# Kernel optimization log

Hardware: AMD Instinct MI355X
Metric: run time of the kernel (lower is better)

## Reference

```python
import jax, jax.numpy as jnp
import numpy as np

D_MODEL = 1024
N_HEADS = 16
B, T = 16, 512


def setup_inputs() -> dict:
    key = jax.random.key(0)
    ks = jax.random.split(key, 5)
    s = 0.02
    return {
        "x": jax.random.normal(ks[0], (B, T, D_MODEL), dtype=jnp.float32),
        "w_qkv": jax.random.normal(ks[1], (D_MODEL, 3 * D_MODEL), dtype=jnp.float32) * s,
        "b_qkv": jax.random.normal(ks[2], (3 * D_MODEL,), dtype=jnp.float32) * s,
        "w_o": jax.random.normal(ks[3], (D_MODEL, D_MODEL), dtype=jnp.float32) * s,
        "b_o": jax.random.normal(ks[4], (D_MODEL,), dtype=jnp.float32) * s,
    }


def reference(x, w_qkv, b_qkv, w_o, b_o):
    Bx, Tx, C = x.shape
    H = N_HEADS
    hd = C // H
    qkv = x @ w_qkv + b_qkv                      # [B,T,3C]
    qkv = qkv.reshape(Bx, Tx, 3, H, hd).transpose(2, 0, 3, 1, 4)  # [3,B,H,T,hd]
    q, k, v = qkv[0], qkv[1], qkv[2]
    # NOTE: original scales by sqrt(C) = sqrt(d_model), not sqrt(head_dim)
    att = jnp.einsum("bhqd,bhkd->bhqk", q, k) / jnp.sqrt(jnp.float32(C))
    causal = jnp.tril(jnp.ones((Tx, Tx), dtype=bool))
    att = jnp.where(causal, att, -jnp.inf)
    att = jax.nn.softmax(att, axis=-1)
    y = jnp.einsum("bhqk,bhkd->bhqd", att, v)    # [B,H,T,hd]
    y = y.transpose(0, 2, 1, 3).reshape(Bx, Tx, C)
    return y @ w_o + b_o
```

## Files before the change

kernel.cpp:

```cpp
#include <hip/hip_runtime.h>
#include <cstddef>


#define B_  16
#define T_  512
#define C_  1024
#define H_  16
#define HD_ 64

typedef __bf16 bf16x8 __attribute__((ext_vector_type(8)));
typedef float  f32x4  __attribute__((ext_vector_type(4)));

__device__ __forceinline__ void gload16(const void* g, void* lds_dst) {
  __builtin_amdgcn_global_load_lds(
      (const __attribute__((address_space(1))) unsigned int*)g,
      (__attribute__((address_space(3))) unsigned int*)lds_dst, 16, 0, 0);
}

__global__ void cvt_kernel(const float* __restrict__ in, __bf16* __restrict__ out, int n) {
  int i = (blockIdx.x * 256 + threadIdx.x) * 8;
  if (i >= n) return;
  float4 f0 = *(const float4*)&in[i];
  float4 f1 = *(const float4*)&in[i + 4];
  bf16x8 o;
  o[0] = (__bf16)f0.x; o[1] = (__bf16)f0.y; o[2] = (__bf16)f0.z; o[3] = (__bf16)f0.w;
  o[4] = (__bf16)f1.x; o[5] = (__bf16)f1.y; o[6] = (__bf16)f1.z; o[7] = (__bf16)f1.w;
  *(bf16x8*)&out[i] = o;
}

__global__ void tconv_kernel(const float* __restrict__ w, __bf16* __restrict__ wt,
                             int K, int N) {
  __shared__ float tile[32][33];
  int tx = threadIdx.x, ty = threadIdx.y;
  int n0 = blockIdx.x * 32, k0 = blockIdx.y * 32;
  #pragma unroll
  for (int i = 0; i < 4; ++i) {
    int r = ty + i * 8;
    tile[r][tx] = w[(size_t)(k0 + r) * N + n0 + tx];
  }
  __syncthreads();
  #pragma unroll
  for (int i = 0; i < 4; ++i) {
    int r = ty + i * 8;
    wt[(size_t)(n0 + r) * K + k0 + tx] = (__bf16)tile[tx][r];
  }
}

__global__ __launch_bounds__(256) void gemmsq_kernel(
    const __bf16* __restrict__ A, const __bf16* __restrict__ BT,
    const float* __restrict__ bias, int K, int NBn,
    __bf16* __restrict__ oq, __bf16* __restrict__ okk, __bf16* __restrict__ ovt)
{
  __shared__ __attribute__((aligned(16))) char lds[32768];
  const int tid = threadIdx.x, lane = tid & 63, wid = tid >> 6;
  const int wm = wid >> 1, wn = wid & 1;
  const int lr = lane & 15, lg = lane >> 4;

  const int cpx = gridDim.x >> 3;
  const int id = (blockIdx.x & 7) * cpx + (blockIdx.x >> 3);
  const int m0 = (id / NBn) * 128, n0 = (id % NBn) * 128;

  const int r8  = wid * 8 + (lane >> 3);
  const int csw = ((lane & 7) ^ (lane >> 3)) * 8;

  auto stage = [&](const __bf16* g, char* dst) {
    #pragma unroll
    for (int i = 0; i < 4; ++i)
      gload16(g + (size_t)(i * 32 + r8) * K + csw, dst + i * 4096 + wid * 1024);
  };
  auto rd = [&](bf16x8* d, const char* buf, int woff) {
    #pragma unroll
    for (int f = 0; f < 4; ++f) {
      const char* rp = buf + (woff + f * 16 + lr) * 128;
      #pragma unroll
      for (int ks = 0; ks < 2; ++ks)
        d[f * 2 + ks] = *(const bf16x8*)(rp + (((ks << 2) + lg) ^ (lr & 7)) * 16);
    }
  };

  f32x4 acc[4][4] = {};
  const int nt = K >> 6;
  const __bf16* gA = A  + (size_t)m0 * K;
  const __bf16* gB = BT + (size_t)n0 * K;
  char* const Ab = lds;
  char* const Bb = lds + 16384;

  stage(gA, Ab);
  stage(gB, Bb);
  asm volatile("s_waitcnt vmcnt(0)\ns_barrier" ::: "memory");

  bf16x8 a[8], b[8];
  for (int t = 0; t < nt; ++t) {
    rd(a, Ab, wm * 64);
    rd(b, Bb, wn * 64);
    asm volatile("s_waitcnt lgkmcnt(0)\ns_barrier" ::: "memory");
    if (t + 1 < nt) {
      stage(gA + (size_t)(t + 1) * 64, Ab);
      stage(gB + (size_t)(t + 1) * 64, Bb);
    }
    __builtin_amdgcn_s_setprio(1);
    #pragma unroll
    for (int mf = 0; mf < 4; ++mf)
      #pragma unroll
      for (int nf = 0; nf < 4; ++nf)
        #pragma unroll
        for (int ks = 0; ks < 2; ++ks)
          acc[mf][nf] = __builtin_amdgcn_mfma_f32_16x16x32_bf16(
              a[mf * 2 + ks], b[nf * 2 + ks], acc[mf][nf], 0, 0, 0);
    __builtin_amdgcn_s_setprio(0);
    asm volatile("s_waitcnt vmcnt(0)\ns_barrier" ::: "memory");
  }

  const float QSC = 0.04508422f;
  #pragma unroll
  for (int nf = 0; nf < 4; ++nf) {
    int n = n0 + wn * 64 + nf * 16 + lr;
    float bv = bias[n];
    int which = n >> 10;
    int h = (n >> 6) & 15, d = n & 63;
    if (which == 2) {
      #pragma unroll
      for (int mf = 0; mf < 4; ++mf) {
        int m = m0 + wm * 64 + mf * 16 + lg * 4;
        int bb = m >> 9, t0 = m & 511;
        ushort4 pk;
        __bf16 e0 = (__bf16)(acc[mf][nf][0] + bv);
        __bf16 e1 = (__bf16)(acc[mf][nf][1] + bv);
        __bf16 e2 = (__bf16)(acc[mf][nf][2] + bv);
        __bf16 e3 = (__bf16)(acc[mf][nf][3] + bv);
        pk.x = *(unsigned short*)&e0; pk.y = *(unsigned short*)&e1;
        pk.z = *(unsigned short*)&e2; pk.w = *(unsigned short*)&e3;
        *(ushort4*)&ovt[(size_t)((bb * H_ + h) * HD_ + d) * T_ + t0] = pk;
      }
    } else {
      __bf16* dst = (which == 0) ? oq : okk;
      const float scl = (which == 0) ? QSC : 1.0f;
      #pragma unroll
      for (int mf = 0; mf < 4; ++mf)
        #pragma unroll
        for (int j = 0; j < 4; ++j) {
          int m = m0 + wm * 64 + mf * 16 + lg * 4 + j;
          int bb = m >> 9, tt = m & 511;
          dst[(size_t)((bb * H_ + h) * T_ + tt) * HD_ + d] =
              (__bf16)((acc[mf][nf][j] + bv) * scl);
        }
    }
  }
}

__global__ __launch_bounds__(256) void gemmsq_o_kernel(
    const __bf16* __restrict__ A, const __bf16* __restrict__ BT,
    const float* __restrict__ bias, int K, int NBn, int N,
    float* __restrict__ out32)
{
  __shared__ __attribute__((aligned(16))) char lds[32768];
  const int tid = threadIdx.x, lane = tid & 63, wid = tid >> 6;
  const int wm = wid >> 1, wn = wid & 1;
  const int lr = lane & 15, lg = lane >> 4;

  const int cpx = gridDim.x >> 3;
  const int id = (blockIdx.x & 7) * cpx + (blockIdx.x >> 3);
  const int m0 = (id / NBn) * 128, n0 = (id % NBn) * 128;

  const int r8  = wid * 8 + (lane >> 3);
  const int csw = ((lane & 7) ^ (lane >> 3)) * 8;

  auto stage = [&](const __bf16* g, char* dst) {
    #pragma unroll
    for (int i = 0; i < 4; ++i)
      gload16(g + (size_t)(i * 32 + r8) * K + csw, dst + i * 4096 + wid * 1024);
  };
  auto rd = [&](bf16x8* d, const char* buf, int woff) {
    #pragma unroll
    for (int f = 0; f < 4; ++f) {
      const char* rp = buf + (woff + f * 16 + lr) * 128;
      #pragma unroll
      for (int ks = 0; ks < 2; ++ks)
        d[f * 2 + ks] = *(const bf16x8*)(rp + (((ks << 2) + lg) ^ (lr & 7)) * 16);
    }
  };

  f32x4 acc[4][4] = {};
  const int nt = K >> 6;
  const __bf16* gA = A  + (size_t)m0 * K;
  const __bf16* gB = BT + (size_t)n0 * K;
  char* const Ab = lds;
  char* const Bb = lds + 16384;

  stage(gA, Ab);
  stage(gB, Bb);
  asm volatile("s_waitcnt vmcnt(0)\ns_barrier" ::: "memory");

  bf16x8 a[8], b[8];
  for (int t = 0; t < nt; ++t) {
    rd(a, Ab, wm * 64);
    rd(b, Bb, wn * 64);
    asm volatile("s_waitcnt lgkmcnt(0)\ns_barrier" ::: "memory");
    if (t + 1 < nt) {
      stage(gA + (size_t)(t + 1) * 64, Ab);
      stage(gB + (size_t)(t + 1) * 64, Bb);
    }
    __builtin_amdgcn_s_setprio(1);
    #pragma unroll
    for (int mf = 0; mf < 4; ++mf)
      #pragma unroll
      for (int nf = 0; nf < 4; ++nf)
        #pragma unroll
        for (int ks = 0; ks < 2; ++ks)
          acc[mf][nf] = __builtin_amdgcn_mfma_f32_16x16x32_bf16(
              a[mf * 2 + ks], b[nf * 2 + ks], acc[mf][nf], 0, 0, 0);
    __builtin_amdgcn_s_setprio(0);
    asm volatile("s_waitcnt vmcnt(0)\ns_barrier" ::: "memory");
  }

  #pragma unroll
  for (int nf = 0; nf < 4; ++nf) {
    int n = n0 + wn * 64 + nf * 16 + lr;
    float bv = bias[n];
    #pragma unroll
    for (int mf = 0; mf < 4; ++mf)
      #pragma unroll
      for (int j = 0; j < 4; ++j) {
        int m = m0 + wm * 64 + mf * 16 + lg * 4 + j;
        out32[(size_t)m * N + n] = acc[mf][nf][j] + bv;
      }
  }
}

__global__ __launch_bounds__(512) void attn_kernel(
    const __bf16* __restrict__ qb, const __bf16* __restrict__ kb,
    const __bf16* __restrict__ vtb, __bf16* __restrict__ y)
{
  extern __shared__ __align__(16) char smem[];
  char* const Ksb = smem;
  char* const Vtb = smem + 65536;
  __bf16* const Ps = (__bf16*)(smem + 131072);

  const int tid = threadIdx.x, lane = tid & 63, w = tid >> 6;
  const int lr = lane & 15, lg = lane >> 4;
  const int bh = blockIdx.x;
  const size_t base = (size_t)bh * T_ * HD_;
  const int b = bh >> 4, h = bh & 15;

  {
    const int rk = tid >> 3;
    const int sk = (tid & 7) ^ (rk & 7);
    const int rv = tid >> 6;
    const int sv = (tid & 63) ^ rv;
    #pragma unroll
    for (int i = 0; i < 8; ++i) {
      gload16(kb  + base + (size_t)(i * 64 + rk) * HD_ + sk * 8,
              Ksb + i * 8192 + w * 1024);
      gload16(vtb + base + (size_t)(i * 8 + rv) * T_ + sv * 8,
              Vtb + i * 8192 + w * 1024);
    }
  }
  asm volatile("s_waitcnt vmcnt(0)\ns_barrier" ::: "memory");

  bf16x8 onesf;
  #pragma unroll
  for (int i = 0; i < 8; ++i) onesf[i] = (__bf16)1.0f;

  #pragma unroll 1
  for (int k = 0; k < 4; ++k) {
    const int G = w + 8 * k;
    const int q0 = G * 16;
    const int cG = G >> 2;

    bf16x8 qf[2];
    #pragma unroll
    for (int s = 0; s < 2; ++s)
      qf[s] = *(const bf16x8*)&qb[base + (size_t)(q0 + lr) * HD_ + s * 32 + lg * 8];

    f32x4 acc[4] = {};
    f32x4 sacc = {};

    for (int c = 0; c <= cG; ++c) {
      f32x4 sc[4] = {};
      __builtin_amdgcn_s_setprio(1);
      #pragma unroll
      for (int s = 0; s < 2; ++s) {
        #pragma unroll
        for (int cc = 0; cc < 4; ++cc) {
          const char* kp = Ksb + (size_t)(c * 64 + cc * 16 + lr) * 128
                               + (((s << 2) + lg) ^ (lr & 7)) * 16;
          bf16x8 kf = *(const bf16x8*)kp;
          sc[cc] = __builtin_amdgcn_mfma_f32_16x16x32_bf16(qf[s], kf, sc[cc], 0, 0, 0);
        }
      }
      __builtin_amdgcn_s_setprio(0);

      #pragma unroll
      for (int cc = 0; cc < 4; ++cc)
        #pragma unroll
        for (int j = 0; j < 4; ++j) {
          float p = exp2f(sc[cc][j]);
          if (c == cG) {
            int kv = c * 64 + cc * 16 + lr;
            int qr = q0 + lg * 4 + j;
            if (kv > qr) p = 0.f;
          }
          Ps[((w * 16) + lg * 4 + j) * 72 + cc * 16 + lr] = (__bf16)p;
        }

      __builtin_amdgcn_s_setprio(1);
      #pragma unroll
      for (int s = 0; s < 2; ++s) {
        bf16x8 pa = *(const bf16x8*)&Ps[((w * 16) + lr) * 72 + s * 32 + lg * 8];
        sacc = __builtin_amdgcn_mfma_f32_16x16x32_bf16(pa, onesf, sacc, 0, 0, 0);
        #pragma unroll
        for (int dd = 0; dd < 4; ++dd) {
          const char* vp = Vtb + (size_t)(dd * 16 + lr) * 1024
                               + (8 * c + (((s << 2) + lg) ^ (lr & 7))) * 16;
          bf16x8 vf = *(const bf16x8*)vp;
          acc[dd] = __builtin_amdgcn_mfma_f32_16x16x32_bf16(pa, vf, acc[dd], 0, 0, 0);
        }
      }
      __builtin_amdgcn_s_setprio(0);
    }

    float inv[4];
    #pragma unroll
    for (int j = 0; j < 4; ++j) inv[j] = 1.f / sacc[j];
    #pragma unroll
    for (int dd = 0; dd < 4; ++dd)
      #pragma unroll
      for (int j = 0; j < 4; ++j) {
        int t = q0 + lg * 4 + j;
        int d = dd * 16 + lr;
        y[((size_t)(b * T_ + t)) * C_ + h * HD_ + d] = (__bf16)(acc[dd][j] * inv[j]);
      }
  }
}

extern "C" void kernel_launch(void* const* d_in, const int* in_sizes, int n_in,
                              void* d_out, int out_size, void* d_ws, size_t ws_size,
                              hipStream_t stream) {
  const float* x    = (const float*)d_in[0];
  const float* wqkv = (const float*)d_in[1];
  const float* bqkv = (const float*)d_in[2];
  const float* wo   = (const float*)d_in[3];
  const float* bo   = (const float*)d_in[4];
  float* out = (float*)d_out;

  char* ws = (char*)d_ws;
  const size_t MB = 1u << 20;
  __bf16* xb    = (__bf16*)(ws);
  __bf16* wqt   = (__bf16*)(ws + 16 * MB);
  __bf16* wot   = (__bf16*)(ws + 22 * MB);
  __bf16* qbuf  = (__bf16*)(ws + 24 * MB);
  __bf16* kbuf  = (__bf16*)(ws + 40 * MB);
  __bf16* vtbuf = (__bf16*)(ws + 56 * MB);
  __bf16* ybuf  = (__bf16*)(ws + 72 * MB);

  (void)hipFuncSetAttribute(reinterpret_cast<const void*>(&attn_kernel),
                            hipFuncAttributeMaxDynamicSharedMemorySize, 149504);

  const int NX = B_ * T_ * C_;
  cvt_kernel<<<NX / (256 * 8), 256, 0, stream>>>(x, xb, NX);
  tconv_kernel<<<dim3(3 * C_ / 32, C_ / 32), dim3(32, 8), 0, stream>>>(wqkv, wqt, C_, 3 * C_);
  tconv_kernel<<<dim3(C_ / 32, C_ / 32), dim3(32, 8), 0, stream>>>(wo, wot, C_, C_);

  gemmsq_kernel<<<1536, 256, 0, stream>>>(
      xb, wqt, bqkv, C_, 24, qbuf, kbuf, vtbuf);

  attn_kernel<<<256, 512, 149504, stream>>>(qbuf, kbuf, vtbuf, ybuf);

  gemmsq_o_kernel<<<512, 256, 0, stream>>>(
      ybuf, wot, bo, C_, 8, C_, out);
}
```

Baseline: 126.6 us.

## Pair mirrored query tiles per wave to balance causal work and share K/V loads

```diff
diff --git a/kernel.cpp b/kernel.cpp
--- a/kernel.cpp
+++ b/kernel.cpp
@@ -234,7 +234,7 @@
   extern __shared__ __align__(16) char smem[];
   char* const Ksb = smem;
   char* const Vtb = smem + 65536;
-  __bf16* const Ps = (__bf16*)(smem + 131072);
+  char* const Psb = smem + 131072;
 
   const int tid = threadIdx.x, lane = tid & 63, w = tid >> 6;
   const int lr = lane & 15, lg = lane >> 4;
@@ -261,75 +261,123 @@
   #pragma unroll
   for (int i = 0; i < 8; ++i) onesf[i] = (__bf16)1.0f;
 
+  char* const PsW0 = Psb + (w * 2 + 0) * 2048;
+  char* const PsW1 = Psb + (w * 2 + 1) * 2048;
+
   #pragma unroll 1
-  for (int k = 0; k < 4; ++k) {
-    const int G = w + 8 * k;
-    const int q0 = G * 16;
-    const int cG = G >> 2;
-
-    bf16x8 qf[2];
-    #pragma unroll
-    for (int s = 0; s < 2; ++s)
-      qf[s] = *(const bf16x8*)&qb[base + (size_t)(q0 + lr) * HD_ + s * 32 + lg * 8];
-
-    f32x4 acc[4] = {};
-    f32x4 sacc = {};
-
-    for (int c = 0; c <= cG; ++c) {
-      f32x4 sc[4] = {};
+  for (int sw = 0; sw < 2; ++sw) {
+    const int GA = sw * 16 + w;
+    const int GB = sw * 16 + 15 - w;
+    const int q0A = GA * 16, q0B = GB * 16;
+    const int cA = GA >> 2, cB = GB >> 2;
+
+    bf16x8 qfA[2], qfB[2];
+    #pragma unroll
+    for (int s = 0; s < 2; ++s) {
+      qfA[s] = *(const bf16x8*)&qb[base + (size_t)(q0A + lr) * HD_ + s * 32 + lg * 8];
+      qfB[s] = *(const bf16x8*)&qb[base + (size_t)(q0B + lr) * HD_ + s * 32 + lg * 8];
+    }
+
+    f32x4 accA[4] = {}, accB[4] = {};
+    f32x4 saccA = {}, saccB = {};
+
+    for (int c = 0; c <= cB; ++c) {
+      const bool actA = (c <= cA);
+
+      bf16x8 kf[2][4];
+      #pragma unroll
+      for (int s = 0; s < 2; ++s)
+        #pragma unroll
+        for (int cc = 0; cc < 4; ++cc)
+          kf[s][cc] = *(const bf16x8*)(Ksb + (size_t)(c * 64 + cc * 16 + lr) * 128
+                                       + (((s << 2) + lg) ^ (lr & 7)) * 16);
+
+      #pragma unroll
+      for (int g = 0; g < 2; ++g) {
+        if (g == 0 && !actA) continue;
+        const bf16x8* qf = (g == 0) ? qfA : qfB;
+        const int q0 = (g == 0) ? q0A : q0B;
+        const int cg = (g == 0) ? cA : cB;
+        char* PsW = (g == 0) ? PsW0 : PsW1;
+
+        f32x4 sc[4] = {};
+        __builtin_amdgcn_s_setprio(1);
+        #pragma unroll
+        for (int s = 0; s < 2; ++s)
+          #pragma unroll
+          for (int cc = 0; cc < 4; ++cc)
+            sc[cc] = __builtin_amdgcn_mfma_f32_16x16x32_bf16(
+                kf[s][cc], qf[s], sc[cc], 0, 0, 0);
+        __builtin_amdgcn_s_setprio(0);
+
+        #pragma unroll
+        for (int cc = 0; cc < 4; ++cc) {
+          float p[4];
+          #pragma unroll
+          for (int j = 0; j < 4; ++j) {
+            float v = exp2f(sc[cc][j]);
+            if (c == cg) {
+              int kv = c * 64 + cc * 16 + lg * 4 + j;
+              if (kv > q0 + lr) v = 0.f;
+            }
+            p[j] = v;
+          }
+          ushort4 pkw;
+          __bf16 e0 = (__bf16)p[0], e1 = (__bf16)p[1];
+          __bf16 e2 = (__bf16)p[2], e3 = (__bf16)p[3];
+          pkw.x = *(unsigned short*)&e0; pkw.y = *(unsigned short*)&e1;
+          pkw.z = *(unsigned short*)&e2; pkw.w = *(unsigned short*)&e3;
+          int g16 = (2 * cc + (lg >> 1)) ^ (lr & 7);
+          *(ushort4*)(PsW + lr * 128 + g16 * 16 + (lg & 1) * 8) = pkw;
+        }
+      }
+
+      bf16x8 vf[2][4];
+      #pragma unroll
+      for (int s = 0; s < 2; ++s)
+        #pragma unroll
+        for (int dd = 0; dd < 4; ++dd)
+          vf[s][dd] = *(const bf16x8*)(Vtb + (size_t)(dd * 16 + lr) * 1024
+                                       + (8 * c + (((s << 2) + lg) ^ (lr & 7))) * 16);
+
       __builtin_amdgcn_s_setprio(1);
       #pragma unroll
-      for (int s = 0; s < 2; ++s) {
-        #pragma unroll
-        for (int cc = 0; cc < 4; ++cc) {
-          const char* kp = Ksb + (size_t)(c * 64 + cc * 16 + lr) * 128
-                               + (((s << 2) + lg) ^ (lr & 7)) * 16;
-          bf16x8 kf = *(const bf16x8*)kp;
-          sc[cc] = __builtin_amdgcn_mfma_f32_16x16x32_bf16(qf[s], kf, sc[cc], 0, 0, 0);
+      for (int g = 0; g < 2; ++g) {
+        if (g == 0 && !actA) continue;
+        char* PsW = (g == 0) ? PsW0 : PsW1;
+        f32x4* acc = (g == 0) ? accA : accB;
+        f32x4& sacc = (g == 0) ? saccA : saccB;
+        #pragma unroll
+        for (int s = 0; s < 2; ++s) {
+          bf16x8 pa = *(const bf16x8*)(PsW + lr * 128
+                                       + (((s << 2) + lg) ^ (lr & 7)) * 16);
+          sacc = __builtin_amdgcn_mfma_f32_16x16x32_bf16(pa, onesf, sacc, 0, 0, 0);
+          #pragma unroll
+          for (int dd = 0; dd < 4; ++dd)
+            acc[dd] = __builtin_amdgcn_mfma_f32_16x16x32_bf16(
+                pa, vf[s][dd], acc[dd], 0, 0, 0);
         }
       }
       __builtin_amdgcn_s_setprio(0);
-
-      #pragma unroll
-      for (int cc = 0; cc < 4; ++cc)
+    }
+
+    #pragma unroll
+    for (int g = 0; g < 2; ++g) {
+      const int q0 = (g == 0) ? q0A : q0B;
+      f32x4* acc = (g == 0) ? accA : accB;
+      f32x4& sacc = (g == 0) ? saccA : saccB;
+      float inv[4];
+      #pragma unroll
+      for (int j = 0; j < 4; ++j) inv[j] = 1.f / sacc[j];
+      #pragma unroll
+      for (int dd = 0; dd < 4; ++dd)
         #pragma unroll
         for (int j = 0; j < 4; ++j) {
-          float p = exp2f(sc[cc][j]);
-          if (c == cG) {
-            int kv = c * 64 + cc * 16 + lr;
-            int qr = q0 + lg * 4 + j;
-            if (kv > qr) p = 0.f;
-          }
-          Ps[((w * 16) + lg * 4 + j) * 72 + cc * 16 + lr] = (__bf16)p;
+          int t = q0 + lg * 4 + j;
+          int d = dd * 16 + lr;
+          y[((size_t)(b * T_ + t)) * C_ + h * HD_ + d] = (__bf16)(acc[dd][j] * inv[j]);
         }
-
-      __builtin_amdgcn_s_setprio(1);
-      #pragma unroll
-      for (int s = 0; s < 2; ++s) {
-        bf16x8 pa = *(const bf16x8*)&Ps[((w * 16) + lr) * 72 + s * 32 + lg * 8];
-        sacc = __builtin_amdgcn_mfma_f32_16x16x32_bf16(pa, onesf, sacc, 0, 0, 0);
-        #pragma unroll
-        for (int dd = 0; dd < 4; ++dd) {
-          const char* vp = Vtb + (size_t)(dd * 16 + lr) * 1024
-                               + (8 * c + (((s << 2) + lg) ^ (lr & 7))) * 16;
-          bf16x8 vf = *(const bf16x8*)vp;
-          acc[dd] = __builtin_amdgcn_mfma_f32_16x16x32_bf16(pa, vf, acc[dd], 0, 0, 0);
-        }
-      }
-      __builtin_amdgcn_s_setprio(0);
-    }
-
-    float inv[4];
-    #pragma unroll
-    for (int j = 0; j < 4; ++j) inv[j] = 1.f / sacc[j];
-    #pragma unroll
-    for (int dd = 0; dd < 4; ++dd)
-      #pragma unroll
-      for (int j = 0; j < 4; ++j) {
-        int t = q0 + lg * 4 + j;
-        int d = dd * 16 + lr;
-        y[((size_t)(b * T_ + t)) * C_ + h * HD_ + d] = (__bf16)(acc[dd][j] * inv[j]);
-      }
+    }
   }
 }
 
@@ -354,7 +402,7 @@
   __bf16* ybuf  = (__bf16*)(ws + 72 * MB);
 
   (void)hipFuncSetAttribute(reinterpret_cast<const void*>(&attn_kernel),
-                            hipFuncAttributeMaxDynamicSharedMemorySize, 149504);
+                            hipFuncAttributeMaxDynamicSharedMemorySize, 163840);
 
   const int NX = B_ * T_ * C_;
   cvt_kernel<<<NX / (256 * 8), 256, 0, stream>>>(x, xb, NX);
@@ -364,7 +412,7 @@
   gemmsq_kernel<<<1536, 256, 0, stream>>>(
       xb, wqt, bqkv, C_, 24, qbuf, kbuf, vtbuf);
 
-  attn_kernel<<<256, 512, 149504, stream>>>(qbuf, kbuf, vtbuf, ybuf);
+  attn_kernel<<<256, 512, 163840, stream>>>(qbuf, kbuf, vtbuf, ybuf);
 
   gemmsq_o_kernel<<<512, 256, 0, stream>>>(
       ybuf, wot, bo, C_, 8, C_, out);
```

Measured after the change: 124.1 us. 1.02x faster.
